# Kernel tuning notes

Measured on AMD Instinct MI355X. Metric: run time of the kernel, lower is better.

The kernel has to match this reference:

```python
import jax, jax.numpy as jnp
import numpy as np
from jax import lax

KS = 3
PAD = 1
N = KS * KS


def setup_inputs() -> dict:
    key = jax.random.key(0)
    k1, k2, k3, k4, k5, k6 = jax.random.split(key, 6)
    b, cin, cout, h, w = 4, 64, 64, 256, 256
    x = jax.random.normal(k1, (b, cin, h, w), jnp.float32)
    # offset-predicting conv: 2*N output channels, 3x3, pad 1
    p_conv_w = 0.1 * jax.random.normal(k2, (2 * N, cin, KS, KS), jnp.float32)
    p_conv_b = jnp.zeros((2 * N,), jnp.float32)
    # main conv applied to the k*k-expanded sampled map (no bias in original)
    conv_w = jax.random.normal(k3, (cout, cin, KS, KS), jnp.float32) / np.sqrt(cin * N)
    bn_gamma = 1.0 + 0.1 * jax.random.normal(k4, (cout,), jnp.float32)
    bn_beta = 0.1 * jax.random.normal(k5, (cout,), jnp.float32)
    return {"x": x, "p_conv_w": p_conv_w, "p_conv_b": p_conv_b,
            "conv_w": conv_w, "bn_gamma": bn_gamma, "bn_beta": bn_beta}


def _deform_conv(x, p_conv_w, p_conv_b, conv_w, bn_gamma, bn_beta):
    b, c, h, w = x.shape
    # offsets: (b, 2N, h, w) -> (b, h, w, 2N)
    offset = lax.conv_general_dilated(x, p_conv_w, (1, 1), ((PAD, PAD), (PAD, PAD)))
    offset = offset + p_conv_b[None, :, None, None]
    offset = jnp.transpose(offset, (0, 2, 3, 1))
    # zero-pad input; sampling coordinates live on the padded grid
    x_pad = jnp.pad(x, ((0, 0), (0, 0), (PAD, PAD), (PAD, PAD)))
    Hp, Wp = h + 2 * PAD, w + 2 * PAD
    # p = p_0 + p_n + offset  (x/y coords each of shape (b,h,w,N))
    r = jnp.arange(-(KS - 1) // 2, KS // 2 + 1, dtype=jnp.float32)  # [-1,0,1]
    pn_x, pn_y = jnp.meshgrid(r, r, indexing="ij")
    pn_x, pn_y = pn_x.reshape(-1), pn_y.reshape(-1)  # (N,)
    p0_x = jnp.arange(1, h + 1, dtype=jnp.float32)[:, None, None]  # (h,1,1)
    p0_y = jnp.arange(1, w + 1, dtype=jnp.float32)[None, :, None]  # (1,w,1)
    p_x = offset[..., :N] + p0_x + pn_x  # (b,h,w,N)
    p_y = offset[..., N:] + p0_y + pn_y
    # integer corner coords (detached / non-differentiable), clamped
    fx = jnp.floor(lax.stop_gradient(p_x))
    fy = jnp.floor(lax.stop_gradient(p_y))
    q_lt_x = jnp.clip(fx, 0, Hp - 1).astype(jnp.int32)
    q_lt_y = jnp.clip(fy, 0, Wp - 1).astype(jnp.int32)
    q_rb_x = jnp.clip(fx + 1, 0, Hp - 1).astype(jnp.int32)
    q_rb_y = jnp.clip(fy + 1, 0, Wp - 1).astype(jnp.int32)
    # clamped continuous coords (gradient flows to offsets)
    px = jnp.clip(p_x, 0, Hp - 1)
    py = jnp.clip(p_y, 0, Wp - 1)
    # bilinear weights
    ltx = q_lt_x.astype(px.dtype); lty = q_lt_y.astype(px.dtype)
    rbx = q_rb_x.astype(px.dtype); rby = q_rb_y.astype(px.dtype)
    g_lt = (1 + (ltx - px)) * (1 + (lty - py))
    g_rb = (1 - (rbx - px)) * (1 - (rby - py))
    g_lb = (1 + (ltx - px)) * (1 - (rby - py))
    g_rt = (1 - (rbx - px)) * (1 + (lty - py))
    x_flat = x_pad.reshape(b, c, Hp * Wp)

    def gather(qx, qy):
        idx = (qx * Wp + qy).reshape(b, 1, -1)  # (b,1,h*w*N)
        out = jnp.take_along_axis(x_flat, idx, axis=2)
        return out.reshape(b, c, h, w, N)

    x_off = (g_lt[:, None] * gather(q_lt_x, q_lt_y)
             + g_rb[:, None] * gather(q_rb_x, q_rb_y)
             + g_lb[:, None] * gather(q_lt_x, q_rb_y)
             + g_rt[:, None] * gather(q_rb_x, q_lt_y))  # (b,c,h,w,N)
    # conv (kernel=KS, stride=KS on k*k-expanded map) == contraction over (c,N)
    out = jnp.einsum("bchwn,ocn->bohw", x_off, conv_w.reshape(conv_w.shape[0], c, N))
    # BatchNorm2d (training-mode batch statistics) + LeakyReLU(0.1)
    mean = out.mean(axis=(0, 2, 3), keepdims=True)
    var = out.var(axis=(0, 2, 3), keepdims=True)
    y = (out - mean) * lax.rsqrt(var + 1e-5)
    y = y * bn_gamma[None, :, None, None] + bn_beta[None, :, None, None]
    return jnp.where(y > 0, y, 0.1 * y)


def reference(x, p_conv_w, p_conv_b, conv_w, bn_gamma, bn_beta):
    return _deform_conv(x, p_conv_w, p_conv_b, conv_w, bn_gamma, bn_beta)
```

## Files before the change

kernel.cpp:

```cpp
#include <hip/hip_runtime.h>
#include <math.h>

#define BB 4
#define CC 64
#define OCC 64
#define HH 256
#define WW 256
#define HP 258
#define WP 258
#define NPIX (BB * HH * WW)
#define CNT_F 262144.0f

typedef __attribute__((ext_vector_type(8))) __bf16 bf16x8;
typedef __attribute__((ext_vector_type(4))) float f32x4;

__device__ __forceinline__ float blo(unsigned u) {
    return __builtin_bit_cast(float, u << 16);
}
__device__ __forceinline__ float bhi(unsigned u) {
    return __builtin_bit_cast(float, u & 0xffff0000u);
}

__global__ __launch_bounds__(256) void pad_transpose(const float* __restrict__ x,
                                                     __bf16* __restrict__ xt) {
    int blk = blockIdx.x;
    int xchunk = blk & 3;
    int y = (blk >> 2) & 255;
    int b = blk >> 10;
    int tid = threadIdx.x;
    __shared__ float tile[64][65];
    int x0 = xchunk * 64;
    int col = tid & 63;
    int crow = tid >> 6;
    const float* xp = x + ((size_t)b * CC) * HH * WW + (size_t)y * WW + x0;
#pragma unroll
    for (int i = 0; i < 16; ++i) {
        int c = crow + i * 4;
        tile[c][col] = xp[(size_t)c * HH * WW + col];
    }
    __syncthreads();
    __bf16* op = xt + (((size_t)b * HP + (y + 1)) * WP + (x0 + 1)) * CC;
#pragma unroll
    for (int i = 0; i < 16; ++i) {
        int xl = crow + i * 4;
        op[(size_t)xl * CC + col] = (__bf16)tile[col][xl];
    }
}

__global__ void zero_border(__bf16* __restrict__ xt) {
    int i = blockIdx.x * 256 + threadIdx.x;
    const int total = BB * 1028 * CC;
    if (i >= total) return;
    int c = i & 63;
    int p = (i >> 6) % 1028;
    int b = (i >> 6) / 1028;
    int yp, xp;
    if (p < 258)      { yp = 0;           xp = p; }
    else if (p < 516) { yp = 257;         xp = p - 258; }
    else if (p < 772) { yp = p - 516 + 1; xp = 0; }
    else              { yp = p - 772 + 1; xp = 257; }
    xt[(((size_t)b * HP + yp) * WP + xp) * CC + c] = (__bf16)0.0f;
}

__global__ void reorder_weights(const float* __restrict__ cw,
                                const float* __restrict__ pw,
                                __bf16* __restrict__ wtb,
                                __bf16* __restrict__ pwb) {
    int i = blockIdx.x * 256 + threadIdx.x;
    if (i < 36864) {
        int c = i & 63;
        int n = (i >> 6) % 9;
        int oc = i / 576;
        wtb[i] = (__bf16)cw[((size_t)oc * CC + c) * 9 + n];
    } else {
        int j = i - 36864;
        if (j >= 18432) return;
        int c = j & 63;
        int n = (j >> 6) % 9;
        int oc = j / 576;
        pwb[j] = (__bf16)(oc < 18 ? pw[((size_t)oc * CC + c) * 9 + n] : 0.0f);
    }
}

__global__ __launch_bounds__(256, 8) void deform_fused(const __bf16* __restrict__ xt,
                                                       const __bf16* __restrict__ pwb,
                                                       const float* __restrict__ pb,
                                                       const __bf16* __restrict__ wtb,
                                                       float* __restrict__ out) {
    int phys = blockIdx.x;
    int blk = (phys & 7) * 2048 + (phys >> 3);
    int xh = blk & 15;
    int y  = (blk >> 4) & 255;
    int b  = blk >> 12;
    int x0 = xh * 16;
    int tid = threadIdx.x;
    int wave = tid >> 6, lane = tid & 63;
    int chp = lane & 31, half = lane >> 5;

    __shared__ __attribute__((aligned(16))) char smem[19584];
    __bf16 (*sS)[18][72] = (__bf16 (*)[18][72])smem;
    char* sAb = smem;
    float* offbuf = (float*)(smem + 18432);

    {
        const char* base = (const char*)xt + (size_t)b * HP * WP * CC * 2;
        for (int t = tid; t < 1728; t += 256) {
            int pos = t >> 5, cp = t & 31;
            int r = pos / 18, j = pos - r * 18;
            unsigned d = *(const unsigned*)(base
                + (size_t)((y + r) * WP + (x0 + j)) * (CC * 2) + cp * 4);
            *(unsigned*)&sS[r][j][cp * 2] = d;
        }
    }
    __syncthreads();

    if (wave < 2) {
        int nh = wave;
        int m = lane & 15, q = lane >> 4;
        f32x4 acc = {0.0f, 0.0f, 0.0f, 0.0f};
        const __bf16* bp = pwb + (size_t)(nh * 16 + m) * 576 + q * 8;
#pragma unroll
        for (int n = 0; n < 9; ++n) {
            int dy = n / 3, dx = n - dy * 3;
            const __bf16* abase = &sS[dy][m + dx][q * 8];
#pragma unroll
            for (int h = 0; h < 2; ++h) {
                bf16x8 a  = *(const bf16x8*)(abase + h * 32);
                bf16x8 bv = *(const bf16x8*)(bp + n * 64 + h * 32);
                acc = __builtin_amdgcn_mfma_f32_16x16x32_bf16(a, bv, acc, 0, 0, 0);
            }
        }
        int oc = nh * 16 + m;
        if (oc < 18) {
            float bias = pb[oc];
#pragma unroll
            for (int r = 0; r < 4; ++r)
                offbuf[(q * 4 + r) * 18 + oc] = acc[r] + bias;
        }
    }
    __syncthreads();

    float g0 = 0.0f, g1 = 0.0f, g2 = 0.0f, g3 = 0.0f;
    int c0 = 0, c1 = 0, c2 = 0, c3 = 0;
    if (lane < 36) {
        int t = wave * 36 + lane;
        int n = t >> 4, p = t & 15;
        float offx = offbuf[p * 18 + n];
        float offy = offbuf[p * 18 + n + 9];
        float px = offx + (float)(y + 1) + (float)(n / 3 - 1);
        float py = offy + (float)(x0 + p + 1) + (float)(n % 3 - 1);
        float fx = floorf(px), fy = floorf(py);
        float pxc = fminf(fmaxf(px, 0.0f), 257.0f);
        float pyc = fminf(fmaxf(py, 0.0f), 257.0f);
        int ltx = (int)fminf(fmaxf(fx, 0.0f), 257.0f);
        int lty = (int)fminf(fmaxf(fy, 0.0f), 257.0f);
        int rbx = (int)fminf(fmaxf(fx + 1.0f, 0.0f), 257.0f);
        int rby = (int)fminf(fmaxf(fy + 1.0f, 0.0f), 257.0f);
        float dxl = 1.0f + ((float)ltx - pxc);
        float dxr = 1.0f - ((float)rbx - pxc);
        float dyl = 1.0f + ((float)lty - pyc);
        float dyr = 1.0f - ((float)rby - pyc);
        g0 = dxl * dyl;
        g1 = dxr * dyr;
        g2 = dxl * dyr;
        g3 = dxr * dyl;
        c0 = ((ltx * WP + lty) * CC) * 2;
        c1 = ((rbx * WP + rby) * CC) * 2;
        c2 = ((ltx * WP + rby) * CC) * 2;
        c3 = ((rbx * WP + lty) * CC) * 2;
    }

    {
        const char* xbl = (const char*)xt + (size_t)b * HP * WP * CC * 2 + (size_t)chp * 4;
#pragma unroll 3
        for (int r = 0; r < 18; ++r) {
            int src = r * 2 + half;
            float gx = __shfl(g0, src, 64);
            float gy = __shfl(g1, src, 64);
            float gz = __shfl(g2, src, 64);
            float gw = __shfl(g3, src, 64);
            int vx = __shfl(c0, src, 64);
            int vy = __shfl(c1, src, 64);
            int vz = __shfl(c2, src, 64);
            int vw = __shfl(c3, src, 64);
            unsigned d0 = *(const unsigned*)(xbl + vx);
            unsigned d1 = *(const unsigned*)(xbl + vy);
            unsigned d2 = *(const unsigned*)(xbl + vz);
            unsigned d3 = *(const unsigned*)(xbl + vw);
            float lo = gx * blo(d0) + gy * blo(d1) + gz * blo(d2) + gw * blo(d3);
            float hi = gx * bhi(d0) + gy * bhi(d1) + gz * bhi(d2) + gw * bhi(d3);
            __bf16 rlo = (__bf16)lo, rhi = (__bf16)hi;
            ushort2 rv;
            rv.x = __builtin_bit_cast(unsigned short, rlo);
            rv.y = __builtin_bit_cast(unsigned short, rhi);
            int t = wave * 36 + src;
            int n = t >> 4, p = t & 15;
            unsigned bo = (unsigned)p * 1152u + (unsigned)n * 128u + (unsigned)chp * 4u;
            bo ^= (unsigned)((p & 7) << 4);
            *(ushort2*)(sAb + bo) = rv;
        }
    }
    __syncthreads();

    int m = lane & 15, q = lane >> 4;
    f32x4 acc = {0.0f, 0.0f, 0.0f, 0.0f};
    {
        unsigned rowb = (unsigned)m * 1152u;
        unsigned key = (unsigned)((m & 7) << 4);
        const __bf16* bp = wtb + (size_t)(wave * 16 + m) * 576 + q * 8;
        __builtin_amdgcn_s_setprio(1);
#pragma unroll
        for (int k0 = 0; k0 < 576; k0 += 32) {
            unsigned bo = rowb + (((unsigned)(k0 * 2 + q * 16)) ^ key);
            bf16x8 a  = *(const bf16x8*)(sAb + bo);
            bf16x8 bv = *(const bf16x8*)(bp + k0);
            acc = __builtin_amdgcn_mfma_f32_16x16x32_bf16(a, bv, acc, 0, 0, 0);
        }
        __builtin_amdgcn_s_setprio(0);
    }

    int oc = wave * 16 + m;
    float* ob = out + (((size_t)b * OCC + oc) * HH + y) * WW + x0 + q * 4;
    float4 v;
    v.x = acc[0]; v.y = acc[1]; v.z = acc[2]; v.w = acc[3];
    *(float4*)ob = v;
}

__global__ __launch_bounds__(256) void stats_kernel(const float* __restrict__ out,
                                                    float* __restrict__ stats) {
    int blk = blockIdx.x;
    int b = blk & 3;
    int oc = blk >> 2;
    const float* p = out + ((size_t)b * OCC + oc) * HH * WW;
    float s = 0.0f, q = 0.0f;
    for (int i = threadIdx.x; i < HH * WW; i += 256) {
        float v = p[i];
        s += v;
        q += v * v;
    }
#pragma unroll
    for (int d = 1; d < 64; d <<= 1) {
        s += __shfl_xor(s, d, 64);
        q += __shfl_xor(q, d, 64);
    }
    __shared__ float sm[8];
    int wave = threadIdx.x >> 6, lane = threadIdx.x & 63;
    if (lane == 0) { sm[wave] = s; sm[4 + wave] = q; }
    __syncthreads();
    if (threadIdx.x == 0) {
        float ts = sm[0] + sm[1] + sm[2] + sm[3];
        float tq = sm[4] + sm[5] + sm[6] + sm[7];
        atomicAdd(&stats[oc], ts);
        atomicAdd(&stats[64 + oc], tq);
    }
}

__global__ __launch_bounds__(256) void bn_leaky(float* __restrict__ out,
                                                const float* __restrict__ stats,
                                                const float* __restrict__ gamma,
                                                const float* __restrict__ beta) {
    int i = blockIdx.x * 256 + threadIdx.x;
    int oc = (i >> 14) & 63;
    float mean = stats[oc] * (1.0f / CNT_F);
    float var = stats[64 + oc] * (1.0f / CNT_F) - mean * mean;
    float scale = gamma[oc] * rsqrtf(var + 1e-5f);
    float shift = beta[oc] - mean * scale;
    float4* o4 = (float4*)out;
    float4 v = o4[i];
    v.x = v.x * scale + shift; v.x = v.x > 0.0f ? v.x : 0.1f * v.x;
    v.y = v.y * scale + shift; v.y = v.y > 0.0f ? v.y : 0.1f * v.y;
    v.z = v.z * scale + shift; v.z = v.z > 0.0f ? v.z : 0.1f * v.z;
    v.w = v.w * scale + shift; v.w = v.w > 0.0f ? v.w : 0.1f * v.w;
    o4[i] = v;
}

extern "C" void kernel_launch(void* const* d_in, const int* in_sizes, int n_in,
                              void* d_out, int out_size, void* d_ws, size_t ws_size,
                              hipStream_t stream) {
    (void)in_sizes; (void)n_in; (void)out_size; (void)ws_size;
    const float* x     = (const float*)d_in[0];
    const float* pw    = (const float*)d_in[1];
    const float* pb    = (const float*)d_in[2];
    const float* cw    = (const float*)d_in[3];
    const float* gamma = (const float*)d_in[4];
    const float* beta  = (const float*)d_in[5];
    float* out = (float*)d_out;
    char* ws = (char*)d_ws;

    __bf16* xtb  = (__bf16*)ws;
    __bf16* wtb  = (__bf16*)(ws + 34080768 + 18874368);
    __bf16* pwb  = (__bf16*)(ws + 34080768 + 18874368 + 73728);
    float*  stats = (float*)(ws + 34080768 + 18874368 + 73728 + 36864);

    hipMemsetAsync(stats, 0, 128 * sizeof(float), stream);
    pad_transpose<<<4096, 256, 0, stream>>>(x, xtb);
    zero_border<<<(BB * 1028 * CC + 255) / 256, 256, 0, stream>>>(xtb);
    reorder_weights<<<216, 256, 0, stream>>>(cw, pw, wtb, pwb);
    deform_fused<<<16384, 256, 0, stream>>>(xtb, pwb, pb, wtb, out);
    stats_kernel<<<OCC * BB, 256, 0, stream>>>(out, stats);
    bn_leaky<<<NPIX * OCC / 4 / 256, 256, 0, stream>>>(out, stats, gamma, beta);
}
```

Before: 438.8 us.

## Merge prep kernels, widen halo loads, split offset conv across four waves

Folds the pad/transpose, border zeroing, weight reorder and stats memset into one prep launch, which removes three kernel launches and a memset. In the fused deform kernel, the halo tile is now loaded with 16-byte vector loads instead of 4-byte ones. The offset-conv MFMA work is split over all four waves by dividing the taps between two wave pairs, with the partial sums added when they are read. This needs a bit more shared memory, so launch bounds drop from 8 to 7 blocks per CU, which may lower occupancy.

```diff
diff --git a/kernel.cpp b/kernel.cpp
--- a/kernel.cpp
+++ b/kernel.cpp
@@ -21,68 +21,70 @@
     return __builtin_bit_cast(float, u & 0xffff0000u);
 }
 
-__global__ __launch_bounds__(256) void pad_transpose(const float* __restrict__ x,
-                                                     __bf16* __restrict__ xt) {
+__global__ __launch_bounds__(256) void prep(const float* __restrict__ x,
+                                            __bf16* __restrict__ xt,
+                                            const float* __restrict__ cw,
+                                            const float* __restrict__ pw,
+                                            __bf16* __restrict__ wtb,
+                                            __bf16* __restrict__ pwb,
+                                            float* __restrict__ stats) {
     int blk = blockIdx.x;
-    int xchunk = blk & 3;
-    int y = (blk >> 2) & 255;
-    int b = blk >> 10;
     int tid = threadIdx.x;
-    __shared__ float tile[64][65];
-    int x0 = xchunk * 64;
-    int col = tid & 63;
-    int crow = tid >> 6;
-    const float* xp = x + ((size_t)b * CC) * HH * WW + (size_t)y * WW + x0;
-#pragma unroll
-    for (int i = 0; i < 16; ++i) {
-        int c = crow + i * 4;
-        tile[c][col] = xp[(size_t)c * HH * WW + col];
-    }
-    __syncthreads();
-    __bf16* op = xt + (((size_t)b * HP + (y + 1)) * WP + (x0 + 1)) * CC;
-#pragma unroll
-    for (int i = 0; i < 16; ++i) {
-        int xl = crow + i * 4;
-        op[(size_t)xl * CC + col] = (__bf16)tile[col][xl];
-    }
-}
-
-__global__ void zero_border(__bf16* __restrict__ xt) {
-    int i = blockIdx.x * 256 + threadIdx.x;
-    const int total = BB * 1028 * CC;
-    if (i >= total) return;
-    int c = i & 63;
-    int p = (i >> 6) % 1028;
-    int b = (i >> 6) / 1028;
-    int yp, xp;
-    if (p < 258)      { yp = 0;           xp = p; }
-    else if (p < 516) { yp = 257;         xp = p - 258; }
-    else if (p < 772) { yp = p - 516 + 1; xp = 0; }
-    else              { yp = p - 772 + 1; xp = 257; }
-    xt[(((size_t)b * HP + yp) * WP + xp) * CC + c] = (__bf16)0.0f;
-}
-
-__global__ void reorder_weights(const float* __restrict__ cw,
-                                const float* __restrict__ pw,
-                                __bf16* __restrict__ wtb,
-                                __bf16* __restrict__ pwb) {
-    int i = blockIdx.x * 256 + threadIdx.x;
-    if (i < 36864) {
+    if (blk < 4096) {
+        int xchunk = blk & 3;
+        int y = (blk >> 2) & 255;
+        int b = blk >> 10;
+        __shared__ float tile[64][65];
+        int x0 = xchunk * 64;
+        int col = tid & 63;
+        int crow = tid >> 6;
+        const float* xp = x + ((size_t)b * CC) * HH * WW + (size_t)y * WW + x0;
+#pragma unroll
+        for (int i = 0; i < 16; ++i) {
+            int c = crow + i * 4;
+            tile[c][col] = xp[(size_t)c * HH * WW + col];
+        }
+        __syncthreads();
+        __bf16* op = xt + (((size_t)b * HP + (y + 1)) * WP + (x0 + 1)) * CC;
+#pragma unroll
+        for (int i = 0; i < 16; ++i) {
+            int xl = crow + i * 4;
+            op[(size_t)xl * CC + col] = (__bf16)tile[col][xl];
+        }
+    } else if (blk < 5124) {
+        int i = (blk - 4096) * 256 + tid;
+        const int total = BB * 1028 * CC;
+        if (i >= total) return;
         int c = i & 63;
-        int n = (i >> 6) % 9;
-        int oc = i / 576;
-        wtb[i] = (__bf16)cw[((size_t)oc * CC + c) * 9 + n];
+        int p = (i >> 6) % 1028;
+        int b = (i >> 6) / 1028;
+        int yp, xp;
+        if (p < 258)      { yp = 0;           xp = p; }
+        else if (p < 516) { yp = 257;         xp = p - 258; }
+        else if (p < 772) { yp = p - 516 + 1; xp = 0; }
+        else              { yp = p - 772 + 1; xp = 257; }
+        xt[(((size_t)b * HP + yp) * WP + xp) * CC + c] = (__bf16)0.0f;
+    } else if (blk < 5340) {
+        int i = (blk - 5124) * 256 + tid;
+        if (i < 36864) {
+            int c = i & 63;
+            int n = (i >> 6) % 9;
+            int oc = i / 576;
+            wtb[i] = (__bf16)cw[((size_t)oc * CC + c) * 9 + n];
+        } else {
+            int j = i - 36864;
+            if (j >= 18432) return;
+            int c = j & 63;
+            int n = (j >> 6) % 9;
+            int oc = j / 576;
+            pwb[j] = (__bf16)(oc < 18 ? pw[((size_t)oc * CC + c) * 9 + n] : 0.0f);
+        }
     } else {
-        int j = i - 36864;
-        if (j >= 18432) return;
-        int c = j & 63;
-        int n = (j >> 6) % 9;
-        int oc = j / 576;
-        pwb[j] = (__bf16)(oc < 18 ? pw[((size_t)oc * CC + c) * 9 + n] : 0.0f);
-    }
-}
-
-__global__ __launch_bounds__(256, 8) void deform_fused(const __bf16* __restrict__ xt,
+        if (tid < 128) stats[tid] = 0.0f;
+    }
+}
+
+__global__ __launch_bounds__(256, 7) void deform_fused(const __bf16* __restrict__ xt,
                                                        const __bf16* __restrict__ pwb,
                                                        const float* __restrict__ pb,
                                                        const __bf16* __restrict__ wtb,
@@ -97,45 +99,61 @@
     int wave = tid >> 6, lane = tid & 63;
     int chp = lane & 31, half = lane >> 5;
 
-    __shared__ __attribute__((aligned(16))) char smem[19584];
+    __shared__ __attribute__((aligned(16))) char smem[20736];
     __bf16 (*sS)[18][72] = (__bf16 (*)[18][72])smem;
     char* sAb = smem;
-    float* offbuf = (float*)(smem + 18432);
+    float* offp = (float*)(smem + 18432);
 
     {
         const char* base = (const char*)xt + (size_t)b * HP * WP * CC * 2;
-        for (int t = tid; t < 1728; t += 256) {
-            int pos = t >> 5, cp = t & 31;
+        for (int t = tid; t < 432; t += 256) {
+            int pos = t >> 3, c8 = t & 7;
             int r = pos / 18, j = pos - r * 18;
-            unsigned d = *(const unsigned*)(base
-                + (size_t)((y + r) * WP + (x0 + j)) * (CC * 2) + cp * 4);
-            *(unsigned*)&sS[r][j][cp * 2] = d;
+            uint4 d = *(const uint4*)(base
+                + (size_t)((y + r) * WP + (x0 + j)) * (CC * 2) + c8 * 16);
+            *(uint4*)&sS[r][j][c8 * 8] = d;
         }
     }
     __syncthreads();
 
-    if (wave < 2) {
-        int nh = wave;
+    {
+        int nh = wave & 1;
+        int kh = wave >> 1;
         int m = lane & 15, q = lane >> 4;
         f32x4 acc = {0.0f, 0.0f, 0.0f, 0.0f};
         const __bf16* bp = pwb + (size_t)(nh * 16 + m) * 576 + q * 8;
-#pragma unroll
-        for (int n = 0; n < 9; ++n) {
-            int dy = n / 3, dx = n - dy * 3;
-            const __bf16* abase = &sS[dy][m + dx][q * 8];
-#pragma unroll
-            for (int h = 0; h < 2; ++h) {
-                bf16x8 a  = *(const bf16x8*)(abase + h * 32);
-                bf16x8 bv = *(const bf16x8*)(bp + n * 64 + h * 32);
-                acc = __builtin_amdgcn_mfma_f32_16x16x32_bf16(a, bv, acc, 0, 0, 0);
+        if (kh == 0) {
+#pragma unroll
+            for (int n = 0; n < 5; ++n) {
+                int dy = n / 3, dx = n - dy * 3;
+                const __bf16* abase = &sS[dy][m + dx][q * 8];
+#pragma unroll
+                for (int h = 0; h < 2; ++h) {
+                    bf16x8 a  = *(const bf16x8*)(abase + h * 32);
+                    bf16x8 bv = *(const bf16x8*)(bp + n * 64 + h * 32);
+                    acc = __builtin_amdgcn_mfma_f32_16x16x32_bf16(a, bv, acc, 0, 0, 0);
+                }
+            }
+        } else {
+#pragma unroll
+            for (int n = 5; n < 9; ++n) {
+                int dy = n / 3, dx = n - dy * 3;
+                const __bf16* abase = &sS[dy][m + dx][q * 8];
+#pragma unroll
+                for (int h = 0; h < 2; ++h) {
+                    bf16x8 a  = *(const bf16x8*)(abase + h * 32);
+                    bf16x8 bv = *(const bf16x8*)(bp + n * 64 + h * 32);
+                    acc = __builtin_amdgcn_mfma_f32_16x16x32_bf16(a, bv, acc, 0, 0, 0);
+                }
             }
         }
         int oc = nh * 16 + m;
         if (oc < 18) {
-            float bias = pb[oc];
+            float bias = (kh == 0) ? pb[oc] : 0.0f;
+            float* obf = offp + kh * 288;
 #pragma unroll
             for (int r = 0; r < 4; ++r)
-                offbuf[(q * 4 + r) * 18 + oc] = acc[r] + bias;
+                obf[(q * 4 + r) * 18 + oc] = acc[r] + bias;
         }
     }
     __syncthreads();
@@ -145,8 +163,8 @@
     if (lane < 36) {
         int t = wave * 36 + lane;
         int n = t >> 4, p = t & 15;
-        float offx = offbuf[p * 18 + n];
-        float offy = offbuf[p * 18 + n + 9];
+        float offx = offp[p * 18 + n]     + offp[288 + p * 18 + n];
+        float offy = offp[p * 18 + n + 9] + offp[288 + p * 18 + n + 9];
         float px = offx + (float)(y + 1) + (float)(n / 3 - 1);
         float py = offy + (float)(x0 + p + 1) + (float)(n % 3 - 1);
         float fx = floorf(px), fy = floorf(py);
@@ -292,10 +310,7 @@
     __bf16* pwb  = (__bf16*)(ws + 34080768 + 18874368 + 73728);
     float*  stats = (float*)(ws + 34080768 + 18874368 + 73728 + 36864);
 
-    hipMemsetAsync(stats, 0, 128 * sizeof(float), stream);
-    pad_transpose<<<4096, 256, 0, stream>>>(x, xtb);
-    zero_border<<<(BB * 1028 * CC + 255) / 256, 256, 0, stream>>>(xtb);
-    reorder_weights<<<216, 256, 0, stream>>>(cw, pw, wtb, pwb);
+    prep<<<5341, 256, 0, stream>>>(x, xtb, cw, pw, wtb, pwb, stats);
     deform_fused<<<16384, 256, 0, stream>>>(xtb, pwb, pb, wtb, out);
     stats_kernel<<<OCC * BB, 256, 0, stream>>>(out, stats);
     bn_leaky<<<NPIX * OCC / 4 / 256, 256, 0, stream>>>(out, stats, gamma, beta);
```

Result: faster. 429.8 us (-2.0%).
